# Kernel tuning notes

Hardware: AMD Instinct MI355X
Metric: run time of the kernel (lower is better)

The kernel has to match this reference:

```python
import jax, jax.numpy as jnp
import numpy as np

KEEP = 0.3  # dropout p = 0.7


def setup_inputs() -> dict:
    key = jax.random.key(0)
    k1, k2, k3, k4 = jax.random.split(key, 4)
    E, N, D = 1000000, 100000, 64
    review_feat = jax.random.normal(k1, (E, D), dtype=jnp.float32)
    ci = jax.random.uniform(k2, (N, 1), dtype=jnp.float32)
    W = jax.random.normal(k3, (D, D), dtype=jnp.float32) * (1.0 / np.sqrt(D))
    # inverted dropout mask on gathered src ci: Bernoulli(keep)/keep, shape [E,1]
    drop_mask = (jax.random.bernoulli(k4, KEEP, (E, 1)).astype(jnp.float32) / KEEP)
    src = jax.random.randint(jax.random.fold_in(key, 10), (E,), 0, N, dtype=jnp.int32)
    dst = jax.random.randint(jax.random.fold_in(key, 11), (E,), 0, N, dtype=jnp.int32)
    return {"review_feat": review_feat, "ci": ci, "W": W,
            "drop_mask": drop_mask, "src": src, "dst": dst}


def reference(review_feat, ci, W, drop_mask, src, dst):
    N = ci.shape[0]
    # edge linear: r = review_feat @ W^T   [E, 64]
    r = jnp.einsum('ed,fd->ef', review_feat, W)
    # message: r * dropout(ci[src])       [E, 64] (ci gathered per edge, [E,1] broadcast)
    m = r * (ci[src] * drop_mask)
    # scatter-sum to destination nodes    [N, 64]
    h = jax.ops.segment_sum(m, dst, num_segments=N)
    # final scale by dst ci
    return h * ci
```

## Files before the change

### kernel.cpp

```cpp
#include <hip/hip_runtime.h>


typedef __attribute__((ext_vector_type(8))) short bf16x8;
typedef __attribute__((ext_vector_type(4))) float f32x4;

static __device__ __forceinline__ short f2bf(float f) {
    union { float f; unsigned u; } v; v.f = f;
    unsigned r = v.u + 0x7FFFu + ((v.u >> 16) & 1u);
    return (short)(r >> 16);
}

__global__ __launch_bounds__(256)
void gcn_scatter(const float* __restrict__ feat,
                 const float* __restrict__ ci,
                 const float* __restrict__ mask,
                 const int*   __restrict__ src,
                 const int*   __restrict__ dst,
                 float* __restrict__ g,
                 int E)
{
    const int lane = threadIdx.x & 63;
    const int wid  = (blockIdx.x * blockDim.x + threadIdx.x) >> 6;
    const int nw   = (gridDim.x * blockDim.x) >> 6;

    for (int base = wid * 64; base < E; base += nw * 64) {
        const int e = base + lane;
        float sv = 0.0f;
        int   db = 0;
        if (e < E) {
            const float m = mask[e];
            if (m != 0.0f) {
                const int id = dst[e];
                sv = ci[src[e]] * m * ci[id];
                db = id * 64;
            }
        }
        unsigned long long alive = __ballot(sv != 0.0f);

        while (alive) {
            const int j0 = __builtin_ctzll(alive);
            alive &= alive - 1;
            int j1 = -1;
            if (alive) { j1 = __builtin_ctzll(alive); alive &= alive - 1; }

            const float s0 = __shfl(sv, j0, 64);
            const int   b0 = __shfl(db, j0, 64);
            const float v0 = feat[(size_t)(base + j0) * 64 + lane];

            float s1 = 0.0f; int b1 = 0; float v1 = 0.0f;
            if (j1 >= 0) {
                s1 = __shfl(sv, j1, 64);
                b1 = __shfl(db, j1, 64);
                v1 = feat[(size_t)(base + j1) * 64 + lane];
            }

            unsafeAtomicAdd(g + b0 + lane, v0 * s0);
            if (j1 >= 0)
                unsafeAtomicAdd(g + b1 + lane, v1 * s1);
        }
    }
}

__global__ __launch_bounds__(256)
void gcn_rowgemm(const float* __restrict__ W,
                 float* __restrict__ g,
                 int N)
{
    const int lane = threadIdx.x & 63;
    const int wave = threadIdx.x >> 6;
    const int r16  = lane & 15;
    const int q    = lane >> 4;

    bf16x8 bfrag[4][2];
#pragma unroll
    for (int t = 0; t < 4; ++t) {
        const float* wrow = W + (t * 16 + r16) * 64;
#pragma unroll
        for (int s = 0; s < 2; ++s) {
            const float4 w0 = *(const float4*)(wrow + s * 32 + q * 8);
            const float4 w1 = *(const float4*)(wrow + s * 32 + q * 8 + 4);
            bf16x8 b;
            b[0] = f2bf(w0.x); b[1] = f2bf(w0.y); b[2] = f2bf(w0.z); b[3] = f2bf(w0.w);
            b[4] = f2bf(w1.x); b[5] = f2bf(w1.y); b[6] = f2bf(w1.z); b[7] = f2bf(w1.w);
            bfrag[t][s] = b;
        }
    }

    const int wid = blockIdx.x * 4 + wave;
    const int nw  = gridDim.x * 4;
    for (int n0 = wid * 16; n0 < N; n0 += nw * 16) {
        int ar = n0 + r16;
        if (ar >= N) ar = N - 1;
        const float* arow = g + (size_t)ar * 64 + q * 8;
        bf16x8 afrag[2];
#pragma unroll
        for (int s = 0; s < 2; ++s) {
            const float4 a0 = *(const float4*)(arow + s * 32);
            const float4 a1 = *(const float4*)(arow + s * 32 + 4);
            bf16x8 a;
            a[0] = f2bf(a0.x); a[1] = f2bf(a0.y); a[2] = f2bf(a0.z); a[3] = f2bf(a0.w);
            a[4] = f2bf(a1.x); a[5] = f2bf(a1.y); a[6] = f2bf(a1.z); a[7] = f2bf(a1.w);
            afrag[s] = a;
        }

        f32x4 acc[4];
#pragma unroll
        for (int t = 0; t < 4; ++t) {
            f32x4 c = {0.f, 0.f, 0.f, 0.f};
            c = __builtin_amdgcn_mfma_f32_16x16x32_bf16(afrag[0], bfrag[t][0], c, 0, 0, 0);
            c = __builtin_amdgcn_mfma_f32_16x16x32_bf16(afrag[1], bfrag[t][1], c, 0, 0, 0);
            acc[t] = c;
        }

#pragma unroll
        for (int r = 0; r < 4; ++r) {
            const int orow = n0 + q * 4 + r;
            if (orow < N) {
#pragma unroll
                for (int t = 0; t < 4; ++t)
                    g[(size_t)orow * 64 + t * 16 + r16] = acc[t][r];
            }
        }
    }
}

extern "C" void kernel_launch(void* const* d_in, const int* in_sizes, int n_in,
                              void* d_out, int out_size, void* d_ws, size_t ws_size,
                              hipStream_t stream) {
    const float* feat = (const float*)d_in[0];
    const float* ci   = (const float*)d_in[1];
    const float* W    = (const float*)d_in[2];
    const float* mask = (const float*)d_in[3];
    const int*   src  = (const int*)d_in[4];
    const int*   dst  = (const int*)d_in[5];
    float* out = (float*)d_out;

    const int E = in_sizes[3];
    const int N = in_sizes[1];

    hipMemsetAsync(d_out, 0, (size_t)out_size * sizeof(float), stream);

    gcn_scatter<<<dim3(2048), dim3(256), 0, stream>>>(feat, ci, mask, src, dst, out, E);
    gcn_rowgemm<<<dim3(1024), dim3(256), 0, stream>>>(W, out, N);
}
```

Measured before the change: 376.6 us.

## Replace atomic scatter with CSR bucketing by destination and per-node gather

Instead of having each live edge atomically add its 64-float message into the destination row, the edges are first bucketed by destination: a histogram pass, a per-wave prefix-sum offset assignment, and a placement pass that records edge ids and scale factors. A gather kernel then has one wave per node sum its incoming edges in registers and write the row once. This removes the float atomics to global memory and the output memset, at the cost of three extra passes over the edge arrays and integer atomics on the counters. Offsets come from an unordered atomic bucket allocation, so the order in which edges are summed is not deterministic.

```diff
diff --git a/kernel.cpp b/kernel.cpp
--- a/kernel.cpp
+++ b/kernel.cpp
@@ -11,53 +11,87 @@
 }
 
 __global__ __launch_bounds__(256)
-void gcn_scatter(const float* __restrict__ feat,
-                 const float* __restrict__ ci,
-                 const float* __restrict__ mask,
-                 const int*   __restrict__ src,
-                 const int*   __restrict__ dst,
-                 float* __restrict__ g,
-                 int E)
+void k_hist(const float* __restrict__ mask, const int* __restrict__ dst,
+            int* __restrict__ cnt, int E)
+{
+    int e = blockIdx.x * blockDim.x + threadIdx.x;
+    const int stride = gridDim.x * blockDim.x;
+    for (; e < E; e += stride) {
+        if (mask[e] != 0.0f) atomicAdd(&cnt[dst[e]], 1);
+    }
+}
+
+__global__ __launch_bounds__(256)
+void k_assign(const int* __restrict__ cnt, int* __restrict__ off,
+              int* __restrict__ pos, int* __restrict__ gtotal, int N)
 {
     const int lane = threadIdx.x & 63;
-    const int wid  = (blockIdx.x * blockDim.x + threadIdx.x) >> 6;
-    const int nw   = (gridDim.x * blockDim.x) >> 6;
+    const int n = blockIdx.x * blockDim.x + threadIdx.x;
 
-    for (int base = wid * 64; base < E; base += nw * 64) {
-        const int e = base + lane;
-        float sv = 0.0f;
-        int   db = 0;
-        if (e < E) {
-            const float m = mask[e];
-            if (m != 0.0f) {
-                const int id = dst[e];
-                sv = ci[src[e]] * m * ci[id];
-                db = id * 64;
-            }
+    int d = (n < N) ? cnt[n] : 0;
+    int s = d;
+#pragma unroll
+    for (int o = 1; o < 64; o <<= 1) {
+        int u = __shfl_up(s, o, 64);
+        if (lane >= o) s += u;
+    }
+    const int total = __shfl(s, 63, 64);
+    int base = 0;
+    if (lane == 63) base = atomicAdd(gtotal, total);
+    base = __shfl(base, 63, 64);
+    const int my = base + s - d;
+    if (n < N) { off[n] = my; pos[n] = my; }
+}
+
+__global__ __launch_bounds__(256)
+void k_place(const float* __restrict__ mask, const float* __restrict__ ci,
+             const int* __restrict__ src, const int* __restrict__ dst,
+             int* __restrict__ pos, int* __restrict__ eid,
+             float* __restrict__ esv, int E)
+{
+    int e = blockIdx.x * blockDim.x + threadIdx.x;
+    const int stride = gridDim.x * blockDim.x;
+    for (; e < E; e += stride) {
+        const float m = mask[e];
+        if (m != 0.0f) {
+            const int id = dst[e];
+            const float sv = ci[src[e]] * m * ci[id];
+            const int p = atomicAdd(&pos[id], 1);
+            eid[p] = e;
+            esv[p] = sv;
         }
-        unsigned long long alive = __ballot(sv != 0.0f);
+    }
+}
 
-        while (alive) {
-            const int j0 = __builtin_ctzll(alive);
-            alive &= alive - 1;
-            int j1 = -1;
-            if (alive) { j1 = __builtin_ctzll(alive); alive &= alive - 1; }
+__global__ __launch_bounds__(256)
+void k_gather(const float* __restrict__ feat, const int* __restrict__ cnt,
+              const int* __restrict__ off, const int* __restrict__ eid,
+              const float* __restrict__ esv, float* __restrict__ g, int N)
+{
+    const int lane = threadIdx.x & 63;
+    int n = (blockIdx.x * blockDim.x + threadIdx.x) >> 6;
+    const int nw = (gridDim.x * blockDim.x) >> 6;
 
-            const float s0 = __shfl(sv, j0, 64);
-            const int   b0 = __shfl(db, j0, 64);
-            const float v0 = feat[(size_t)(base + j0) * 64 + lane];
+    for (; n < N; n += nw) {
+        const int d = cnt[n];
+        const int o = off[n];
+        float h = 0.0f;
+        for (int p = 0; p < d; p += 4) {
+            const int rem = d - p;
+            const int   e0 = eid[o + p];
+            const float s0 = esv[o + p];
+            int e1 = 0, e2 = 0, e3 = 0;
+            float s1 = 0.f, s2 = 0.f, s3 = 0.f;
+            if (rem > 1) { e1 = eid[o + p + 1]; s1 = esv[o + p + 1]; }
+            if (rem > 2) { e2 = eid[o + p + 2]; s2 = esv[o + p + 2]; }
+            if (rem > 3) { e3 = eid[o + p + 3]; s3 = esv[o + p + 3]; }
 
-            float s1 = 0.0f; int b1 = 0; float v1 = 0.0f;
-            if (j1 >= 0) {
-                s1 = __shfl(sv, j1, 64);
-                b1 = __shfl(db, j1, 64);
-                v1 = feat[(size_t)(base + j1) * 64 + lane];
-            }
-
-            unsafeAtomicAdd(g + b0 + lane, v0 * s0);
-            if (j1 >= 0)
-                unsafeAtomicAdd(g + b1 + lane, v1 * s1);
+            h += s0 * feat[(size_t)e0 * 64 + lane];
+            if (rem > 1) h += s1 * feat[(size_t)e1 * 64 + lane];
+            if (rem > 2) h += s2 * feat[(size_t)e2 * 64 + lane];
+            if (rem > 3) h += s3 * feat[(size_t)e3 * 64 + lane];
         }
+        g[(size_t)n * 64 + lane] = h;
     }
 }
 
@@ -138,8 +172,18 @@
     const int E = in_sizes[3];
     const int N = in_sizes[1];
 
-    hipMemsetAsync(d_out, 0, (size_t)out_size * sizeof(float), stream);
+    int*   cnt    = (int*)d_ws;
+    int*   gtotal = cnt + N;
+    int*   off    = gtotal + 1;
+    int*   pos    = off + N;
+    int*   eid    = pos + N;
+    float* esv    = (float*)(eid + E);
 
-    gcn_scatter<<<dim3(2048), dim3(256), 0, stream>>>(feat, ci, mask, src, dst, out, E);
+    hipMemsetAsync(d_ws, 0, (size_t)(N + 1) * sizeof(int), stream);
+
+    k_hist  <<<dim3(2048), dim3(256), 0, stream>>>(mask, dst, cnt, E);
+    k_assign<<<dim3((N + 255) / 256), dim3(256), 0, stream>>>(cnt, off, pos, gtotal, N);
+    k_place <<<dim3(2048), dim3(256), 0, stream>>>(mask, ci, src, dst, pos, eid, esv, E);
+    k_gather<<<dim3((N + 3) / 4), dim3(256), 0, stream>>>(feat, cnt, off, eid, esv, out, N);
     gcn_rowgemm<<<dim3(1024), dim3(256), 0, stream>>>(W, out, N);
 }
```

Result: slower. 439.6 us (+16.7%).
